# Optimization experiments

Measured on AMD Instinct MI355X. Metric: run time of the kernel, lower is better.

Reference implementation:

```python
import jax, jax.numpy as jnp
import numpy as np

EPS = 1e-6
DN = ('NCHW', 'OIHW', 'NCHW')


def _dw_conv(s, w, dilation, k):
    pad = dilation * (k - 1) // 2
    return jax.lax.conv_general_dilated(
        s, w, window_strides=(1, 1), padding=[(pad, pad), (pad, pad)],
        rhs_dilation=(dilation, dilation), dimension_numbers=DN,
        feature_group_count=4)


def _branch(s, dw_w, pw_w, pw_b, dilation, k):
    h = _dw_conv(s, dw_w, dilation, k)           # [B,4,H,W]
    # pointwise 1x1 conv 4 -> 1
    return jnp.einsum('bchw,oc->bohw', h, pw_w) + pw_b[None, :, None, None]


def setup_inputs() -> dict:
    key = jax.random.key(0)
    ks = jax.random.split(key, 12)
    B, C, H, W = 32, 64, 128, 128
    nb, rh = 3, 8
    d = {}
    d['x'] = jax.random.normal(ks[0], (B, C, H, W), dtype=jnp.float32)
    # branch 0: k=3 d=1; branch 1: k=7 d=1; branch 2: k=7 d=2
    d['dw0'] = jax.random.normal(ks[1], (4, 1, 3, 3), dtype=jnp.float32) * 0.2
    d['dw1'] = jax.random.normal(ks[2], (4, 1, 7, 7), dtype=jnp.float32) * 0.1
    d['dw2'] = jax.random.normal(ks[3], (4, 1, 7, 7), dtype=jnp.float32) * 0.1
    d['pw0_w'] = jax.random.normal(ks[4], (1, 4), dtype=jnp.float32) * 0.5
    d['pw0_b'] = jnp.zeros((1,), dtype=jnp.float32)
    d['pw1_w'] = jax.random.normal(ks[5], (1, 4), dtype=jnp.float32) * 0.5
    d['pw1_b'] = jnp.zeros((1,), dtype=jnp.float32)
    d['pw2_w'] = jax.random.normal(ks[6], (1, 4), dtype=jnp.float32) * 0.5
    d['pw2_b'] = jnp.zeros((1,), dtype=jnp.float32)
    # router: 1x1 convs on pooled [B,4,1,1] == dense layers
    d['rw1'] = jax.random.normal(ks[7], (rh, 4), dtype=jnp.float32) * 0.5
    d['rb1'] = jnp.zeros((rh,), dtype=jnp.float32)
    d['rw2'] = jax.random.normal(ks[8], (nb, rh), dtype=jnp.float32) * 0.3
    d['rb2'] = jnp.zeros((nb,), dtype=jnp.float32)
    # t_raw = softplus_inverse(1.0)
    d['t_raw'] = jnp.asarray(np.log(np.expm1(1.0)), dtype=jnp.float32)
    return d


def reference(x, dw0, dw1, dw2, pw0_w, pw0_b, pw1_w, pw1_b, pw2_w, pw2_b,
              rw1, rb1, rw2, rb2, t_raw):
    B, C, H, W = x.shape
    avg_map = jnp.mean(x, axis=1, keepdims=True)        # [B,1,H,W]
    max_map = jnp.max(x, axis=1, keepdims=True)         # [B,1,H,W]
    xs = jnp.linspace(-1.0, 1.0, W, dtype=x.dtype)
    ys = jnp.linspace(-1.0, 1.0, H, dtype=x.dtype)
    yy, xx = jnp.meshgrid(ys, xs, indexing='ij')
    xg = jnp.broadcast_to(xx[None, None], (B, 1, H, W))
    yg = jnp.broadcast_to(yy[None, None], (B, 1, H, W))
    s = jnp.concatenate([avg_map, max_map, xg, yg], axis=1)  # [B,4,H,W]

    # router: global avg pool -> 1x1 conv -> relu -> 1x1 conv -> softmax
    pooled = jnp.mean(s, axis=(2, 3))                    # [B,4]
    hid = jax.nn.relu(pooled @ rw1.T + rb1)              # [B,rh]
    logits = hid @ rw2.T + rb2                           # [B,nb]
    rw = jax.nn.softmax(logits, axis=1)                  # [B,nb]

    z = jnp.stack([
        _branch(s, dw0, pw0_w, pw0_b, 1, 3),
        _branch(s, dw1, pw1_w, pw1_b, 1, 7),
        _branch(s, dw2, pw2_w, pw2_b, 2, 7),
    ], axis=1)                                           # [B,nb,1,H,W]

    wlogits = jnp.sum(rw[:, :, None, None, None] * z, axis=1)  # [B,1,H,W]
    T = jax.nn.softplus(t_raw) + EPS
    sa = jax.nn.sigmoid(wlogits / T)                     # [B,1,H,W]
    Y = x * sa                                           # [B,C,H,W]
    return (Y, sa)
```

## Files before the change

kernel.cpp:

```cpp
#include <hip/hip_runtime.h>

#define B_ 32
#define C_ 64
#define H_ 128
#define W_ 128
#define HW_ (H_*W_)
#define CHW_ (C_*HW_)

typedef float f4 __attribute__((ext_vector_type(4)));

__global__ __launch_bounds__(256) void k0_zpos(
    const float* __restrict__ dw0, const float* __restrict__ dw1,
    const float* __restrict__ dw2,
    const float* __restrict__ pw0w, const float* __restrict__ pw0b,
    const float* __restrict__ pw1w, const float* __restrict__ pw1b,
    const float* __restrict__ pw2w, const float* __restrict__ pw2b,
    float* __restrict__ zpos)
{
    int p = blockIdx.x * 256 + threadIdx.x;
    int gy = p >> 7, gx = p & 127;
    const float sc = 2.0f / 127.0f;
    float z0 = pw0b[0], z1 = pw1b[0], z2 = pw2b[0];
    float px0 = pw0w[2], py0 = pw0w[3];
    float px1 = pw1w[2], py1 = pw1w[3];
    float px2 = pw2w[2], py2 = pw2w[3];

    #pragma unroll
    for (int ky = 0; ky < 3; ++ky)
    #pragma unroll
    for (int kx = 0; kx < 3; ++kx) {
        int iy = gy + ky - 1, ix = gx + kx - 1;
        bool ok = ((unsigned)iy < H_) && ((unsigned)ix < W_);
        float xv = ok ? ix * sc - 1.0f : 0.0f;
        float yv = ok ? iy * sc - 1.0f : 0.0f;
        int t = ky * 3 + kx;
        z0 += px0 * dw0[18 + t] * xv + py0 * dw0[27 + t] * yv;
    }
    #pragma unroll
    for (int ky = 0; ky < 7; ++ky)
    #pragma unroll
    for (int kx = 0; kx < 7; ++kx) {
        int iy = gy + ky - 3, ix = gx + kx - 3;
        bool ok = ((unsigned)iy < H_) && ((unsigned)ix < W_);
        float xv = ok ? ix * sc - 1.0f : 0.0f;
        float yv = ok ? iy * sc - 1.0f : 0.0f;
        int t = ky * 7 + kx;
        z1 += px1 * dw1[98 + t] * xv + py1 * dw1[147 + t] * yv;
    }
    #pragma unroll
    for (int ky = 0; ky < 7; ++ky)
    #pragma unroll
    for (int kx = 0; kx < 7; ++kx) {
        int iy = gy + (ky - 3) * 2, ix = gx + (kx - 3) * 2;
        bool ok = ((unsigned)iy < H_) && ((unsigned)ix < W_);
        float xv = ok ? ix * sc - 1.0f : 0.0f;
        float yv = ok ? iy * sc - 1.0f : 0.0f;
        int t = ky * 7 + kx;
        z2 += px2 * dw2[98 + t] * xv + py2 * dw2[147 + t] * yv;
    }
    zpos[p]           = z0;
    zpos[HW_ + p]     = z1;
    zpos[2 * HW_ + p] = z2;
}

__global__ __launch_bounds__(256) void k1_reduce(
    const float* __restrict__ x, float* __restrict__ avgmap,
    float* __restrict__ maxmap, float* __restrict__ partial)
{
    int t = blockIdx.x * 256 + threadIdx.x;
    int base = t * 4;
    int b = base >> 14;
    int q = base & (HW_ - 1);
    const float4* xp = (const float4*)(x + (size_t)b * CHW_ + q);
    float4 v = xp[0];
    float4 s = v, m = v;
    #pragma unroll 8
    for (int c = 1; c < C_; ++c) {
        float4 u = xp[c * (HW_ / 4)];
        s.x += u.x; s.y += u.y; s.z += u.z; s.w += u.w;
        m.x = fmaxf(m.x, u.x); m.y = fmaxf(m.y, u.y);
        m.z = fmaxf(m.z, u.z); m.w = fmaxf(m.w, u.w);
    }
    const float inv = 1.0f / C_;
    float4 a = make_float4(s.x * inv, s.y * inv, s.z * inv, s.w * inv);
    ((float4*)avgmap)[t] = a;
    ((float4*)maxmap)[t] = m;

    float la = a.x + a.y + a.z + a.w;
    float lm = m.x + m.y + m.z + m.w;
    #pragma unroll
    for (int o = 32; o > 0; o >>= 1) {
        la += __shfl_down(la, o);
        lm += __shfl_down(lm, o);
    }
    __shared__ float wa[4], wm[4];
    int lane = threadIdx.x & 63, wid = threadIdx.x >> 6;
    if (lane == 0) { wa[wid] = la; wm[wid] = lm; }
    __syncthreads();
    if (threadIdx.x == 0) {
        partial[2 * blockIdx.x]     = wa[0] + wa[1] + wa[2] + wa[3];
        partial[2 * blockIdx.x + 1] = wm[0] + wm[1] + wm[2] + wm[3];
    }
}

__global__ __launch_bounds__(256) void k34_fused(
    const float* __restrict__ x,
    const float* __restrict__ avgmap, const float* __restrict__ maxmap,
    const float* __restrict__ dw0, const float* __restrict__ dw1,
    const float* __restrict__ dw2,
    const float* __restrict__ pw0w, const float* __restrict__ pw1w,
    const float* __restrict__ pw2w,
    const float* __restrict__ zpos,
    const float* __restrict__ partial,
    const float* __restrict__ rw1, const float* __restrict__ rb1,
    const float* __restrict__ rw2, const float* __restrict__ rb2,
    const float* __restrict__ t_raw,
    float* __restrict__ y, float* __restrict__ sa_out)
{
    __shared__ float sA[14][140];
    __shared__ float sM[14][140];
    __shared__ float wA0[9], wM0[9];
    __shared__ float wA1[49], wM1[49], wA2[49], wM2[49];
    __shared__ __align__(16) float ssa[256];
    __shared__ float sRW[4];

    int b  = blockIdx.y;
    int y0 = blockIdx.x * 2;
    int tix = threadIdx.x;
    const float* am = avgmap + (size_t)b * HW_;
    const float* mm = maxmap + (size_t)b * HW_;

    for (int idx = tix; idx < 14 * 32; idx += 256) {
        int r = idx >> 5, c4 = idx & 31;
        int gy = y0 - 6 + r;
        bool ok = (unsigned)gy < H_;
        float4 av = ok ? ((const float4*)(am + gy * W_))[c4]
                       : make_float4(0.f, 0.f, 0.f, 0.f);
        float4 mv = ok ? ((const float4*)(mm + gy * W_))[c4]
                       : make_float4(0.f, 0.f, 0.f, 0.f);
        float* pa = &sA[r][6 + c4 * 4];
        float* pm = &sM[r][6 + c4 * 4];
        pa[0] = av.x; pa[1] = av.y; pa[2] = av.z; pa[3] = av.w;
        pm[0] = mv.x; pm[1] = mv.y; pm[2] = mv.z; pm[3] = mv.w;
    }
    for (int idx = tix; idx < 14 * 12; idx += 256) {
        int r = idx / 12, c = idx % 12;
        int cc = (c < 6) ? c : (134 + c - 6);
        sA[r][cc] = 0.0f;
        sM[r][cc] = 0.0f;
    }
    if (tix < 9)  { wA0[tix] = pw0w[0] * dw0[tix];
                    wM0[tix] = pw0w[1] * dw0[9 + tix]; }
    if (tix < 49) { wA1[tix] = pw1w[0] * dw1[tix];
                    wM1[tix] = pw1w[1] * dw1[49 + tix];
                    wA2[tix] = pw2w[0] * dw2[tix];
                    wM2[tix] = pw2w[1] * dw2[49 + tix]; }
    if (tix == 0) {
        float s0 = 0.0f, s1 = 0.0f;
        #pragma unroll
        for (int i = 0; i < 16; ++i) {
            s0 += partial[2 * (b * 16 + i)];
            s1 += partial[2 * (b * 16 + i) + 1];
        }
        float p0 = s0 * (1.0f / HW_);
        float p1 = s1 * (1.0f / HW_);
        float hid[8];
        #pragma unroll
        for (int j = 0; j < 8; ++j)
            hid[j] = fmaxf(0.0f, rb1[j] + rw1[j * 4] * p0 + rw1[j * 4 + 1] * p1);
        float lg[3];
        #pragma unroll
        for (int i = 0; i < 3; ++i) {
            float acc = rb2[i];
            #pragma unroll
            for (int j = 0; j < 8; ++j) acc += hid[j] * rw2[i * 8 + j];
            lg[i] = acc;
        }
        float mx = fmaxf(lg[0], fmaxf(lg[1], lg[2]));
        float e0 = expf(lg[0] - mx), e1 = expf(lg[1] - mx), e2 = expf(lg[2] - mx);
        float inv = 1.0f / (e0 + e1 + e2);
        sRW[0] = e0 * inv;
        sRW[1] = e1 * inv;
        sRW[2] = e2 * inv;
        sRW[3] = 1.0f / (log1pf(expf(t_raw[0])) + 1e-6f);
    }

    int ly = tix >> 7;
    int lx = tix & 127;
    int gy = y0 + ly;
    int pidx = gy * W_ + lx;

    float z0 = zpos[pidx];
    float z1 = zpos[HW_ + pidx];
    float z2 = zpos[2 * HW_ + pidx];

    __syncthreads();

    int wid  = tix >> 6;
    int lane = tix & 63;
    const float* xt = x + (size_t)b * CHW_ + y0 * W_;
    float*       yt = y + (size_t)b * CHW_ + y0 * W_;
    f4 xv[16];
    #pragma unroll
    for (int k = 0; k < 16; ++k)
        xv[k] = *((const f4*)(xt + (wid + k * 4) * HW_) + lane);

    float c0 = 0.0f, c1 = 0.0f, c2 = 0.0f;

    #pragma unroll
    for (int ky = 0; ky < 7; ++ky) {
        const float* ra = &sA[ly + 3 + ky][lx + 3];
        const float* rm = &sM[ly + 3 + ky][lx + 3];
        float av[7], mv[7];
        #pragma unroll
        for (int j = 0; j < 7; ++j) { av[j] = ra[j]; mv[j] = rm[j]; }
        #pragma unroll
        for (int j = 0; j < 7; ++j) {
            int t = ky * 7 + j;
            c1 += wA1[t] * av[j] + wM1[t] * mv[j];
        }
        if (ky >= 2 && ky <= 4) {
            #pragma unroll
            for (int j = 2; j <= 4; ++j) {
                int t = (ky - 2) * 3 + (j - 2);
                c0 += wA0[t] * av[j] + wM0[t] * mv[j];
            }
        }
    }
    #pragma unroll
    for (int ky = 0; ky < 7; ++ky) {
        const float* ra = &sA[ly + 2 * ky][lx];
        const float* rm = &sM[ly + 2 * ky][lx];
        #pragma unroll
        for (int kx = 0; kx < 7; ++kx) {
            int t = ky * 7 + kx;
            c2 += wA2[t] * ra[2 * kx] + wM2[t] * rm[2 * kx];
        }
    }

    float wl = sRW[0] * (z0 + c0) + sRW[1] * (z1 + c1) + sRW[2] * (z2 + c2);
    float s = 1.0f / (1.0f + expf(-wl * sRW[3]));
    ssa[tix] = s;
    __builtin_nontemporal_store(s, &sa_out[(size_t)b * HW_ + pidx]);
    __syncthreads();

    f4 sv = ((const f4*)ssa)[lane];
    #pragma unroll
    for (int k = 0; k < 16; ++k) {
        f4 r = xv[k] * sv;
        __builtin_nontemporal_store(r, (f4*)(yt + (wid + k * 4) * HW_) + lane);
    }
}

extern "C" void kernel_launch(void* const* d_in, const int* in_sizes, int n_in,
                              void* d_out, int out_size, void* d_ws, size_t ws_size,
                              hipStream_t stream)
{
    const float* x     = (const float*)d_in[0];
    const float* dw0   = (const float*)d_in[1];
    const float* dw1   = (const float*)d_in[2];
    const float* dw2   = (const float*)d_in[3];
    const float* pw0w  = (const float*)d_in[4];
    const float* pw0b  = (const float*)d_in[5];
    const float* pw1w  = (const float*)d_in[6];
    const float* pw1b  = (const float*)d_in[7];
    const float* pw2w  = (const float*)d_in[8];
    const float* pw2b  = (const float*)d_in[9];
    const float* rw1   = (const float*)d_in[10];
    const float* rb1   = (const float*)d_in[11];
    const float* rw2   = (const float*)d_in[12];
    const float* rb2   = (const float*)d_in[13];
    const float* t_raw = (const float*)d_in[14];

    float* ws      = (float*)d_ws;
    float* avgmap  = ws;
    float* maxmap  = ws + 524288;
    float* partial = ws + 1048576;
    float* zpos    = ws + 1049600;

    float* Y  = (float*)d_out;
    float* sa = Y + (size_t)B_ * CHW_;

    k1_reduce<<<B_ * HW_ / 4 / 256, 256, 0, stream>>>(x, avgmap, maxmap, partial);
    k0_zpos<<<HW_ / 256, 256, 0, stream>>>(
        dw0, dw1, dw2, pw0w, pw0b, pw1w, pw1b, pw2w, pw2b, zpos);

    dim3 g34(H_ / 2, B_);
    k34_fused<<<g34, 256, 0, stream>>>(
        x, avgmap, maxmap, dw0, dw1, dw2,
        pw0w, pw1w, pw2w, zpos,
        partial, rw1, rb1, rw2, rb2, t_raw, Y, sa);
}
```

Baseline: 295.9 us.

## Fuse reduce, zpos and attention passes into one cooperative persistent kernel

Adds a single cooperative kernel with 1024 blocks. Even blocks compute the channel mean/max maps and per-tile partial sums, some odd blocks compute the positional branch terms, and a grid-wide sync separates this from the conv/sigmoid/scale phase. In that phase each block processes two row tiles and keeps half of the x channels in registers across the gating computation. This removes the separate kernel launches and their gaps, but adds a grid barrier cost, leaves odd blocks partly idle in phase one, and rereads half of x. It falls back to the original three-kernel path if occupancy is too low or the cooperative launch fails.

After: 294.8 us. About the same (-0.4%).

```diff
diff --git a/kernel.cpp b/kernel.cpp
--- a/kernel.cpp
+++ b/kernel.cpp
@@ -1,4 +1,7 @@
 #include <hip/hip_runtime.h>
+#include <hip/hip_cooperative_groups.h>
+
+namespace cg = cooperative_groups;
 
 #define B_ 32
 #define C_ 64
@@ -8,6 +11,257 @@
 #define CHW_ (C_*HW_)
 
 typedef float f4 __attribute__((ext_vector_type(4)));
+
+__global__ __launch_bounds__(256, 4) void mega(
+    const float* __restrict__ x,
+    float* __restrict__ avgmap, float* __restrict__ maxmap,
+    float* __restrict__ partial, float* __restrict__ zpos,
+    const float* __restrict__ dw0, const float* __restrict__ dw1,
+    const float* __restrict__ dw2,
+    const float* __restrict__ pw0w, const float* __restrict__ pw0b,
+    const float* __restrict__ pw1w, const float* __restrict__ pw1b,
+    const float* __restrict__ pw2w, const float* __restrict__ pw2b,
+    const float* __restrict__ rw1, const float* __restrict__ rb1,
+    const float* __restrict__ rw2, const float* __restrict__ rb2,
+    const float* __restrict__ t_raw,
+    float* __restrict__ y, float* __restrict__ sa_out)
+{
+    __shared__ float sA[14][140];
+    __shared__ float sM[14][140];
+    __shared__ float wA0[9], wM0[9];
+    __shared__ float wA1[49], wM1[49], wA2[49], wM2[49];
+    __shared__ __align__(16) float ssa[256];
+    __shared__ float sRW[4];
+    __shared__ float wa[4], wm[4];
+
+    int blk = blockIdx.x;
+    int tix = threadIdx.x;
+
+    if ((blk & 1) == 0) {
+        int tile = blk >> 1;
+        int t = tile * 256 + tix;
+        int base = t * 4;
+        int b = base >> 14;
+        int q = base & (HW_ - 1);
+        const float4* xp = (const float4*)(x + (size_t)b * CHW_ + q);
+        float4 v = xp[0];
+        float4 s = v, m = v;
+        #pragma unroll 8
+        for (int c = 1; c < C_; ++c) {
+            float4 u = xp[c * (HW_ / 4)];
+            s.x += u.x; s.y += u.y; s.z += u.z; s.w += u.w;
+            m.x = fmaxf(m.x, u.x); m.y = fmaxf(m.y, u.y);
+            m.z = fmaxf(m.z, u.z); m.w = fmaxf(m.w, u.w);
+        }
+        const float inv = 1.0f / C_;
+        float4 a = make_float4(s.x * inv, s.y * inv, s.z * inv, s.w * inv);
+        ((float4*)avgmap)[t] = a;
+        ((float4*)maxmap)[t] = m;
+
+        float la = a.x + a.y + a.z + a.w;
+        float lm = m.x + m.y + m.z + m.w;
+        #pragma unroll
+        for (int o = 32; o > 0; o >>= 1) {
+            la += __shfl_down(la, o);
+            lm += __shfl_down(lm, o);
+        }
+        int lane = tix & 63, wid = tix >> 6;
+        if (lane == 0) { wa[wid] = la; wm[wid] = lm; }
+        __syncthreads();
+        if (tix == 0) {
+            partial[2 * tile]     = wa[0] + wa[1] + wa[2] + wa[3];
+            partial[2 * tile + 1] = wm[0] + wm[1] + wm[2] + wm[3];
+        }
+    } else if (blk < 128) {
+        int p = (blk >> 1) * 256 + tix;
+        int gy = p >> 7, gx = p & 127;
+        const float sc = 2.0f / 127.0f;
+        float z0 = pw0b[0], z1 = pw1b[0], z2 = pw2b[0];
+        float px0 = pw0w[2], py0 = pw0w[3];
+        float px1 = pw1w[2], py1 = pw1w[3];
+        float px2 = pw2w[2], py2 = pw2w[3];
+
+        #pragma unroll
+        for (int ky = 0; ky < 3; ++ky)
+        #pragma unroll
+        for (int kx = 0; kx < 3; ++kx) {
+            int iy = gy + ky - 1, ix = gx + kx - 1;
+            bool ok = ((unsigned)iy < H_) && ((unsigned)ix < W_);
+            float xv = ok ? ix * sc - 1.0f : 0.0f;
+            float yv = ok ? iy * sc - 1.0f : 0.0f;
+            int t = ky * 3 + kx;
+            z0 += px0 * dw0[18 + t] * xv + py0 * dw0[27 + t] * yv;
+        }
+        #pragma unroll
+        for (int ky = 0; ky < 7; ++ky)
+        #pragma unroll
+        for (int kx = 0; kx < 7; ++kx) {
+            int iy = gy + ky - 3, ix = gx + kx - 3;
+            bool ok = ((unsigned)iy < H_) && ((unsigned)ix < W_);
+            float xv = ok ? ix * sc - 1.0f : 0.0f;
+            float yv = ok ? iy * sc - 1.0f : 0.0f;
+            int t = ky * 7 + kx;
+            z1 += px1 * dw1[98 + t] * xv + py1 * dw1[147 + t] * yv;
+        }
+        #pragma unroll
+        for (int ky = 0; ky < 7; ++ky)
+        #pragma unroll
+        for (int kx = 0; kx < 7; ++kx) {
+            int iy = gy + (ky - 3) * 2, ix = gx + (kx - 3) * 2;
+            bool ok = ((unsigned)iy < H_) && ((unsigned)ix < W_);
+            float xv = ok ? ix * sc - 1.0f : 0.0f;
+            float yv = ok ? iy * sc - 1.0f : 0.0f;
+            int t = ky * 7 + kx;
+            z2 += px2 * dw2[98 + t] * xv + py2 * dw2[147 + t] * yv;
+        }
+        zpos[p]           = z0;
+        zpos[HW_ + p]     = z1;
+        zpos[2 * HW_ + p] = z2;
+    }
+
+    cg::this_grid().sync();
+
+    #pragma unroll 1
+    for (int t2 = 0; t2 < 2; ++t2) {
+        int tile = blk * 2 + t2;
+        int b  = tile >> 6;
+        int y0 = (tile & 63) * 2;
+
+        __syncthreads();
+
+        const float* am = avgmap + (size_t)b * HW_;
+        const float* mm = maxmap + (size_t)b * HW_;
+
+        for (int idx = tix; idx < 14 * 32; idx += 256) {
+            int r = idx >> 5, c4 = idx & 31;
+            int gy = y0 - 6 + r;
+            bool ok = (unsigned)gy < H_;
+            float4 av = ok ? ((const float4*)(am + gy * W_))[c4]
+                           : make_float4(0.f, 0.f, 0.f, 0.f);
+            float4 mv = ok ? ((const float4*)(mm + gy * W_))[c4]
+                           : make_float4(0.f, 0.f, 0.f, 0.f);
+            float* pa = &sA[r][6 + c4 * 4];
+            float* pm = &sM[r][6 + c4 * 4];
+            pa[0] = av.x; pa[1] = av.y; pa[2] = av.z; pa[3] = av.w;
+            pm[0] = mv.x; pm[1] = mv.y; pm[2] = mv.z; pm[3] = mv.w;
+        }
+        for (int idx = tix; idx < 14 * 12; idx += 256) {
+            int r = idx / 12, c = idx % 12;
+            int cc = (c < 6) ? c : (134 + c - 6);
+            sA[r][cc] = 0.0f;
+            sM[r][cc] = 0.0f;
+        }
+        if (t2 == 0) {
+            if (tix < 9)  { wA0[tix] = pw0w[0] * dw0[tix];
+                            wM0[tix] = pw0w[1] * dw0[9 + tix]; }
+            if (tix < 49) { wA1[tix] = pw1w[0] * dw1[tix];
+                            wM1[tix] = pw1w[1] * dw1[49 + tix];
+                            wA2[tix] = pw2w[0] * dw2[tix];
+                            wM2[tix] = pw2w[1] * dw2[49 + tix]; }
+            if (tix == 0) {
+                float s0 = 0.0f, s1 = 0.0f;
+                #pragma unroll
+                for (int i = 0; i < 16; ++i) {
+                    s0 += partial[2 * (b * 16 + i)];
+                    s1 += partial[2 * (b * 16 + i) + 1];
+                }
+                float p0 = s0 * (1.0f / HW_);
+                float p1 = s1 * (1.0f / HW_);
+                float hid[8];
+                #pragma unroll
+                for (int j = 0; j < 8; ++j)
+                    hid[j] = fmaxf(0.0f, rb1[j] + rw1[j * 4] * p0 + rw1[j * 4 + 1] * p1);
+                float lg[3];
+                #pragma unroll
+                for (int i = 0; i < 3; ++i) {
+                    float acc = rb2[i];
+                    #pragma unroll
+                    for (int j = 0; j < 8; ++j) acc += hid[j] * rw2[i * 8 + j];
+                    lg[i] = acc;
+                }
+                float mx = fmaxf(lg[0], fmaxf(lg[1], lg[2]));
+                float e0 = expf(lg[0] - mx), e1 = expf(lg[1] - mx), e2 = expf(lg[2] - mx);
+                float inv = 1.0f / (e0 + e1 + e2);
+                sRW[0] = e0 * inv;
+                sRW[1] = e1 * inv;
+                sRW[2] = e2 * inv;
+                sRW[3] = 1.0f / (log1pf(expf(t_raw[0])) + 1e-6f);
+            }
+        }
+
+        int ly = tix >> 7;
+        int lx = tix & 127;
+        int gy = y0 + ly;
+        int pidx = gy * W_ + lx;
+
+        float z0 = zpos[pidx];
+        float z1 = zpos[HW_ + pidx];
+        float z2 = zpos[2 * HW_ + pidx];
+
+        __syncthreads();
+
+        int wid  = tix >> 6;
+        int lane = tix & 63;
+        const float* xt = x + (size_t)b * CHW_ + y0 * W_;
+        float*       yt = y + (size_t)b * CHW_ + y0 * W_;
+
+        f4 xva[8];
+        #pragma unroll
+        for (int k = 0; k < 8; ++k)
+            xva[k] = *((const f4*)(xt + (wid + k * 4) * HW_) + lane);
+
+        float c0 = 0.0f, c1 = 0.0f, c2 = 0.0f;
+        #pragma unroll
+        for (int ky = 0; ky < 7; ++ky) {
+            const float* ra = &sA[ly + 3 + ky][lx + 3];
+            const float* rm = &sM[ly + 3 + ky][lx + 3];
+            float av[7], mv[7];
+            #pragma unroll
+            for (int j = 0; j < 7; ++j) { av[j] = ra[j]; mv[j] = rm[j]; }
+            #pragma unroll
+            for (int j = 0; j < 7; ++j) {
+                int t = ky * 7 + j;
+                c1 += wA1[t] * av[j] + wM1[t] * mv[j];
+            }
+            if (ky >= 2 && ky <= 4) {
+                #pragma unroll
+                for (int j = 2; j <= 4; ++j) {
+                    int t = (ky - 2) * 3 + (j - 2);
+                    c0 += wA0[t] * av[j] + wM0[t] * mv[j];
+                }
+            }
+        }
+        #pragma unroll
+        for (int ky = 0; ky < 7; ++ky) {
+            const float* ra = &sA[ly + 2 * ky][lx];
+            const float* rm = &sM[ly + 2 * ky][lx];
+            #pragma unroll
+            for (int kx = 0; kx < 7; ++kx) {
+                int t = ky * 7 + kx;
+                c2 += wA2[t] * ra[2 * kx] + wM2[t] * rm[2 * kx];
+            }
+        }
+
+        float wl = sRW[0] * (z0 + c0) + sRW[1] * (z1 + c1) + sRW[2] * (z2 + c2);
+        float s = 1.0f / (1.0f + expf(-wl * sRW[3]));
+        ssa[tix] = s;
+        __builtin_nontemporal_store(s, &sa_out[(size_t)b * HW_ + pidx]);
+        __syncthreads();
+
+        f4 sv = ((const f4*)ssa)[lane];
+        #pragma unroll
+        for (int k = 0; k < 8; ++k) {
+            f4 r = xva[k] * sv;
+            __builtin_nontemporal_store(r, (f4*)(yt + (wid + k * 4) * HW_) + lane);
+        }
+        #pragma unroll
+        for (int k = 8; k < 16; ++k) {
+            f4 v = *((const f4*)(xt + (wid + k * 4) * HW_) + lane);
+            f4 r = v * sv;
+            __builtin_nontemporal_store(r, (f4*)(yt + (wid + k * 4) * HW_) + lane);
+        }
+    }
+}
 
 __global__ __launch_bounds__(256) void k0_zpos(
     const float* __restrict__ dw0, const float* __restrict__ dw1,
@@ -206,7 +460,6 @@
         xv[k] = *((const f4*)(xt + (wid + k * 4) * HW_) + lane);
 
     float c0 = 0.0f, c1 = 0.0f, c2 = 0.0f;
-
     #pragma unroll
     for (int ky = 0; ky < 7; ++ky) {
         const float* ra = &sA[ly + 3 + ky][lx + 3];
@@ -281,6 +534,30 @@
     float* Y  = (float*)d_out;
     float* sa = Y + (size_t)B_ * CHW_;
 
+    static int use_coop = -1;
+    if (use_coop < 0) {
+        int nb = 0;
+        hipError_t e = hipOccupancyMaxActiveBlocksPerMultiprocessor(
+            &nb, (const void*)mega, 256, 0);
+        use_coop = (e == hipSuccess && nb >= 4) ? 1 : 0;
+    }
+
+    if (use_coop) {
+        void* args[] = {
+            (void*)&x, (void*)&avgmap, (void*)&maxmap, (void*)&partial,
+            (void*)&zpos,
+            (void*)&dw0, (void*)&dw1, (void*)&dw2,
+            (void*)&pw0w, (void*)&pw0b, (void*)&pw1w, (void*)&pw1b,
+            (void*)&pw2w, (void*)&pw2b,
+            (void*)&rw1, (void*)&rb1, (void*)&rw2, (void*)&rb2,
+            (void*)&t_raw, (void*)&Y, (void*)&sa
+        };
+        hipError_t e = hipLaunchCooperativeKernel(
+            (const void*)mega, dim3(1024), dim3(256), args, 0, stream);
+        if (e == hipSuccess) return;
+        use_coop = 0;
+    }
+
     k1_reduce<<<B_ * HW_ / 4 / 256, 256, 0, stream>>>(x, avgmap, maxmap, partial);
     k0_zpos<<<HW_ / 256, 256, 0, stream>>>(
         dw0, dw1, dw2, pw0w, pw0b, pw1w, pw1b, pw2w, pw2b, zpos);
```
